# Optimization experiments

Hardware: AMD Instinct MI355X
Metric: run time of the kernel (lower is better)

## Reference

```python
import jax, jax.numpy as jnp
from jax import lax
import numpy as np

K = 3          # kernel_size
PAD = 1        # K // 2
MAX_OFFSET = 0.1
EPS = 1e-8


def setup_inputs() -> dict:
    key = jax.random.key(0)
    k0, k1, k2 = jax.random.split(key, 3)
    B, C, H, W = 4, 64, 256, 256
    Cmid = C // 4
    x = jax.random.normal(k0, (B, C, H, W), jnp.float32)
    # offset_predictor: Conv2d(C+9, C//4, 3, pad=1) -> LeakyReLU(0.2) -> Conv2d(C//4, 2, 3, pad=1) -> Tanh
    w1 = jax.random.normal(k1, (Cmid, C + K * K, 3, 3), jnp.float32) * 0.05
    b1 = jnp.zeros((Cmid,), jnp.float32)
    w2 = jax.random.normal(k2, (2, Cmid, 3, 3), jnp.float32) * 0.05
    b2 = jnp.zeros((2,), jnp.float32)
    return {"x": x, "w1": w1, "b1": b1, "w2": w2, "b2": b2}


def _conv2d(x, w, b):
    # NCHW, OIHW, stride 1, pad 1 (SAME for 3x3)
    out = lax.conv_general_dilated(x, w, (1, 1), ((PAD, PAD), (PAD, PAD)),
                                   dimension_numbers=("NCHW", "OIHW", "NCHW"))
    return out + b[None, :, None, None]


def _local_cosine_similarity(x):
    # F.unfold with zero padding: neighbors[k] at spatial shift (di-1, dj-1), row-major k = di*K + dj
    B, C, H, W = x.shape
    xp = jnp.pad(x, ((0, 0), (0, 0), (PAD, PAD), (PAD, PAD)))
    neighbors = jnp.stack([xp[:, :, di:di + H, dj:dj + W]
                           for di in range(K) for dj in range(K)], axis=2)  # (B,C,9,H,W)
    center = x[:, :, None, :, :]                                            # (B,C,1,H,W)
    numerator = jnp.sum(neighbors * center, axis=1)                         # (B,9,H,W)
    center_norm = jnp.sqrt(jnp.sum(x * x, axis=1)) + EPS                    # (B,H,W)
    neighbor_norm = jnp.sqrt(jnp.sum(neighbors * neighbors, axis=1)) + EPS  # (B,9,H,W)
    return numerator / (center_norm[:, None] * neighbor_norm)               # (B,9,H,W)


def _grid_sample_border(x, grid):
    # bilinear, padding_mode='border', align_corners=True; grid: (B,H,W,2) with (gx,gy) in [-1,1]
    B, C, H, W = x.shape
    ix = (grid[..., 0] + 1.0) * 0.5 * (W - 1)
    iy = (grid[..., 1] + 1.0) * 0.5 * (H - 1)
    ix = jnp.clip(ix, 0.0, W - 1)
    iy = jnp.clip(iy, 0.0, H - 1)
    x0f = jnp.floor(ix); y0f = jnp.floor(iy)
    wx = ix - x0f; wy = iy - y0f
    x0 = x0f.astype(jnp.int32); y0 = y0f.astype(jnp.int32)
    x1 = jnp.minimum(x0 + 1, W - 1); y1 = jnp.minimum(y0 + 1, H - 1)

    def gather(img, yy, xx):  # img (C,H,W), yy/xx (H,W) -> (C,H,W)
        return img[:, yy, xx]

    g = jax.vmap(gather)
    v00 = g(x, y0, x0); v01 = g(x, y0, x1)
    v10 = g(x, y1, x0); v11 = g(x, y1, x1)
    wx = wx[:, None]; wy = wy[:, None]  # broadcast over channel dim
    return ((1 - wy) * ((1 - wx) * v00 + wx * v01)
            + wy * ((1 - wx) * v10 + wx * v11))


def reference(x, w1, b1, w2, b2):
    B, C, H, W = x.shape
    sim = _local_cosine_similarity(x)                       # (B,9,H,W)
    features = jnp.concatenate([x, sim], axis=1)            # (B,C+9,H,W)
    h = _conv2d(features, w1, b1)
    h = jnp.where(h >= 0, h, 0.2 * h)                       # LeakyReLU(0.2)
    offset = jnp.tanh(_conv2d(h, w2, b2)) * MAX_OFFSET      # (B,2,H,W)
    gy, gx = jnp.meshgrid(jnp.linspace(-1.0, 1.0, H),
                          jnp.linspace(-1.0, 1.0, W), indexing="ij")
    base_grid = jnp.stack([gx, gy], axis=-1)[None]          # (1,H,W,2)
    offset_grid = base_grid + jnp.transpose(offset, (0, 2, 3, 1))
    return _grid_sample_border(x, offset_grid)
```

## Files before the change

kernel.cpp:

```cpp
#include <hip/hip_runtime.h>
#include <math.h>

#define B 4
#define C 64
#define H 256
#define W 256
#define CMID 16
#define CIN 73
#define HW (H*W)
#define NW (CIN*9*CMID)
#define XS_STRIDE 260
#define XSR 258
#define PLN 258

__global__ void transpose_w1_kernel(const float* __restrict__ w1, float* __restrict__ wt) {
    int tid = blockIdx.x * blockDim.x + threadIdx.x;
    if (tid >= NW) return;
    int co = tid & (CMID - 1);
    int rest = tid >> 4;
    int ci = rest / 9;
    int k = rest - ci * 9;
    wt[tid] = w1[(co * CIN + ci) * 9 + k];
}

__device__ __forceinline__ void read_patch9(const float* __restrict__ base, float v[9]) {
#pragma unroll
    for (int r = 0; r < 3; ++r) {
        v[r * 3 + 0] = base[r * XSR + 0];
        v[r * 3 + 1] = base[r * XSR + 1];
        v[r * 3 + 2] = base[r * XSR + 2];
    }
}

__global__ __launch_bounds__(256) void sim_kernel(const float* __restrict__ x,
                                                  float* __restrict__ sim) {
    __shared__ float xs[2][4][3 * XSR];

    int bid = blockIdx.x;
    int sb = (bid & 7) * 128 + (bid >> 3);
    int b = sb >> 8;
    int y = sb & 255;
    int tid = threadIdx.x;

    const float* xb = x + (size_t)b * C * HW;

    bool rv[3];
    long off[3];
#pragma unroll
    for (int j = 0; j < 3; ++j) {
        int grow = y - 1 + j;
        rv[j] = (grow >= 0) && (grow < H);
        off[j] = (long)grow * W + tid;
    }

    if (tid < 48) {
        int e = tid & 1;
        int r = (tid >> 1) % 3;
        int q = (tid >> 1) / 3;
        (&xs[0][0][0])[q * (3 * XSR) + r * XSR + (e ? 257 : 0)] = 0.f;
    }

    float dot[9], nsq[9];
    float csq = 0.f;
#pragma unroll
    for (int i = 0; i < 9; ++i) { dot[i] = nsq[i] = 0.f; }

    float p[12];
#pragma unroll
    for (int k = 0; k < 4; ++k)
#pragma unroll
        for (int j = 0; j < 3; ++j)
            p[k * 3 + j] = rv[j] ? xb[(size_t)k * HW + off[j]] : 0.f;

    int cur = 0;
#pragma unroll 1
    for (int cc = 0; cc < C; cc += 4) {
#pragma unroll
        for (int k = 0; k < 4; ++k)
#pragma unroll
            for (int j = 0; j < 3; ++j)
                xs[cur][k][j * XSR + 1 + tid] = p[k * 3 + j];
        __syncthreads();

        if (cc + 4 < C) {
#pragma unroll
            for (int k = 0; k < 4; ++k)
#pragma unroll
                for (int j = 0; j < 3; ++j)
                    p[k * 3 + j] = rv[j] ? xb[(size_t)(cc + 4 + k) * HW + off[j]] : 0.f;
        }

#pragma unroll
        for (int k = 0; k < 4; ++k) {
            float v[9];
            read_patch9(&xs[cur][k][tid], v);
            float cv = v[4];
            csq = fmaf(cv, cv, csq);
#pragma unroll
            for (int kk = 0; kk < 9; ++kk) {
                if (kk == 4) continue;
                dot[kk] = fmaf(cv, v[kk], dot[kk]);
                nsq[kk] = fmaf(v[kk], v[kk], nsq[kk]);
            }
        }
        cur ^= 1;
    }

    dot[4] = csq;
    nsq[4] = csq;
    float cn = sqrtf(csq) + 1e-8f;
    float* so = sim + (size_t)b * 9 * HW + (size_t)y * W + tid;
#pragma unroll
    for (int kk = 0; kk < 9; ++kk)
        so[(size_t)kk * HW] = dot[kk] / (cn * (sqrtf(nsq[kk]) + 1e-8f));
}

__device__ __forceinline__ void conv1_co4(const float* __restrict__ pl, int l,
                                          int aL, int aR,
                                          const float4 wv[9], float4 acc[2][4]) {
    float v[4][6];
#pragma unroll
    for (int r = 0; r < 4; ++r) {
        const float* rp = pl + r * PLN;
        v[r][1] = rp[l];
        v[r][2] = rp[64 + l];
        v[r][3] = rp[128 + l];
        v[r][4] = rp[192 + l];
        v[r][0] = rp[aL];
        v[r][5] = rp[aR];
    }
#pragma unroll
    for (int kr = 0; kr < 3; ++kr)
#pragma unroll
        for (int kc = 0; kc < 3; ++kc) {
            float4 w = wv[kr * 3 + kc];
#pragma unroll
            for (int rr = 0; rr < 2; ++rr)
#pragma unroll
                for (int cc = 0; cc < 4; ++cc) {
                    float a = v[rr + kr][cc + kc];
                    acc[rr][cc].x = fmaf(a, w.x, acc[rr][cc].x);
                    acc[rr][cc].y = fmaf(a, w.y, acc[rr][cc].y);
                    acc[rr][cc].z = fmaf(a, w.z, acc[rr][cc].z);
                    acc[rr][cc].w = fmaf(a, w.w, acc[rr][cc].w);
                }
        }
}

__global__ __launch_bounds__(256) void conv1_kernel(const float* __restrict__ x,
                                                    const float* __restrict__ sim,
                                                    const float* __restrict__ wt,
                                                    const float* __restrict__ b1,
                                                    float* __restrict__ h) {
    __shared__ float xs[2][2][4 * PLN];

    int tid = threadIdx.x;
    int l = tid & 63;
    int wid = tid >> 6;
    int bid = blockIdx.x;
    int sb = (bid & 7) * 64 + (bid >> 3);
    int b  = sb >> 7;
    int y0 = (sb & 127) << 1;

    int vz;
    asm volatile("v_mov_b32 %0, 0" : "=v"(vz));
    const float4* wq = (const float4*)wt + vz;

    const float* gx = x + (size_t)b * C * HW;
    const float* gs = sim + (size_t)b * 9 * HW;

    int grow = y0 - 1 + wid;
    bool rvw = (grow >= 0) && (grow < H);
    size_t goff = (size_t)grow * W + 4 * l;

    int aL = (l == 0)  ? 256 : 191 + l;
    int aR = (l == 63) ? 257 : l + 1;

    if (tid < 32) {
        int bu = tid >> 4, ch = (tid >> 3) & 1, r = (tid >> 1) & 3, e = tid & 1;
        xs[bu][ch][r * PLN + 256 + e] = 0.f;
    }

    float4 bias = ((const float4*)b1)[wid];
    float4 acc[2][4];
#pragma unroll
    for (int rr = 0; rr < 2; ++rr)
#pragma unroll
        for (int cc = 0; cc < 4; ++cc) acc[rr][cc] = bias;

    float4 wA[9], wB[9];
#pragma unroll
    for (int k = 0; k < 9; ++k) wA[k] = wq[k * 4 + wid];

    float4 p0 = make_float4(0.f, 0.f, 0.f, 0.f), p1 = p0;
    if (rvw) {
        p0 = *(const float4*)(gx + goff);
        p1 = *(const float4*)(gx + HW + goff);
    }

    int cur = 0;
#pragma unroll 1
    for (int cc2 = 0; cc2 < 72; cc2 += 2) {
        {
            float* d0 = &xs[cur][0][wid * PLN];
            d0[l] = p0.x; d0[64 + l] = p0.y; d0[128 + l] = p0.z; d0[192 + l] = p0.w;
            float* d1 = &xs[cur][1][wid * PLN];
            d1[l] = p1.x; d1[64 + l] = p1.y; d1[128 + l] = p1.z; d1[192 + l] = p1.w;
        }
        __syncthreads();

        {
            int ci = cc2 + 2;
            p0 = make_float4(0.f, 0.f, 0.f, 0.f);
            if (rvw)
                p0 = (ci < C) ? *(const float4*)(gx + (size_t)ci * HW + goff)
                              : *(const float4*)(gs + (size_t)(ci - C) * HW + goff);
            int cj = cc2 + 3;
            p1 = make_float4(0.f, 0.f, 0.f, 0.f);
            if (rvw && cj < CIN)
                p1 = (cj < C) ? *(const float4*)(gx + (size_t)cj * HW + goff)
                              : *(const float4*)(gs + (size_t)(cj - C) * HW + goff);
        }

#pragma unroll
        for (int k = 0; k < 9; ++k) wB[k] = wq[((cc2 + 1) * 9 + k) * 4 + wid];

        conv1_co4(&xs[cur][0][0], l, aL, aR, wA, acc);

#pragma unroll
        for (int k = 0; k < 9; ++k) wA[k] = wq[((cc2 + 2) * 9 + k) * 4 + wid];

        conv1_co4(&xs[cur][1][0], l, aL, aR, wB, acc);

        cur ^= 1;
    }

    {
        float* d0 = &xs[cur][0][wid * PLN];
        d0[l] = p0.x; d0[64 + l] = p0.y; d0[128 + l] = p0.z; d0[192 + l] = p0.w;
    }
    __syncthreads();
    conv1_co4(&xs[cur][0][0], l, aL, aR, wA, acc);

    float* ho = h + ((size_t)b * CMID + 4 * wid) * HW + (size_t)y0 * W + 4 * l;
#pragma unroll
    for (int rr = 0; rr < 2; ++rr)
#pragma unroll
        for (int j = 0; j < 4; ++j) {
            float4 o;
            o.x = ((const float*)&acc[rr][0])[j];
            o.y = ((const float*)&acc[rr][1])[j];
            o.z = ((const float*)&acc[rr][2])[j];
            o.w = ((const float*)&acc[rr][3])[j];
            o.x = o.x >= 0.f ? o.x : 0.2f * o.x;
            o.y = o.y >= 0.f ? o.y : 0.2f * o.y;
            o.z = o.z >= 0.f ? o.z : 0.2f * o.z;
            o.w = o.w >= 0.f ? o.w : 0.2f * o.w;
            *(float4*)(ho + (size_t)j * HW + (size_t)rr * W) = o;
        }
}

__device__ __forceinline__ void read_patch_lds(const float* __restrict__ xsbuf,
                                               int rl, int px, float v[3][4]) {
    const float* pb = xsbuf + rl * XS_STRIDE + px;
#pragma unroll
    for (int r = 0; r < 3; ++r) {
        float2 p0 = *(const float2*)(pb + r * XS_STRIDE);
        float2 p1 = *(const float2*)(pb + r * XS_STRIDE + 2);
        v[r][0] = p0.x; v[r][1] = p0.y; v[r][2] = p1.x; v[r][3] = p1.y;
    }
}

__global__ __launch_bounds__(256) void offset_kernel(const float* __restrict__ h,
                                                     const float* __restrict__ w2,
                                                     const float* __restrict__ b2,
                                                     float2* __restrict__ off_buf) {
    __shared__ float lw2[CMID * 9 * 2];
    __shared__ float xs[2][4 * XS_STRIDE];

    int tid = threadIdx.x;
    for (int i = tid; i < CMID * 9 * 2; i += 256) {
        int co = i & 1;
        int rest = i >> 1;
        int ci = rest / 9;
        int kk = rest - ci * 9;
        lw2[i] = w2[(co * CMID + ci) * 9 + kk];
    }

    int bid = blockIdx.x;
    int sb = (bid & 7) * 64 + (bid >> 3);
    int b  = sb >> 7;
    int y0 = (sb & 127) << 1;
    int srow = tid >> 6;
    int sx4  = (tid & 63) << 2;
    int rl = tid >> 7;
    int px = (tid & 127) << 1;
    int y  = y0 + rl;

    int grow = y0 - 1 + srow;
    bool gvalid = (grow >= 0) && (grow < H);
    const float* gh = h + (size_t)b * CMID * HW + (size_t)grow * W + sx4;

    if (tid < 16) {
        int bu = tid >> 3, r = (tid >> 1) & 3, e = (tid & 1) ? 257 : 0;
        xs[bu][r * XS_STRIDE + e] = 0.f;
    }

    float s0x = b2[0], s0y = b2[1], s1x = b2[0], s1y = b2[1];

    float4 r4 = make_float4(0.f, 0.f, 0.f, 0.f);
    if (gvalid) r4 = *(const float4*)gh;

    int cur = 0;
#pragma unroll 1
    for (int ci = 0; ci < CMID; ++ci) {
        float* dst = &xs[cur][srow * XS_STRIDE + 1 + sx4];
        dst[0] = r4.x; dst[1] = r4.y; dst[2] = r4.z; dst[3] = r4.w;
        __syncthreads();
        if (ci + 1 < CMID) {
            r4 = make_float4(0.f, 0.f, 0.f, 0.f);
            if (gvalid) r4 = *(const float4*)(gh + (size_t)(ci + 1) * HW);
        }
        float v[3][4];
        read_patch_lds(xs[cur], rl, px, v);
#pragma unroll
        for (int kr = 0; kr < 3; ++kr)
#pragma unroll
            for (int kc = 0; kc < 3; ++kc) {
                float2 wv = *(const float2*)(lw2 + (ci * 9 + kr * 3 + kc) * 2);
                s0x = fmaf(v[kr][kc],     wv.x, s0x);
                s0y = fmaf(v[kr][kc],     wv.y, s0y);
                s1x = fmaf(v[kr][kc + 1], wv.x, s1x);
                s1y = fmaf(v[kr][kc + 1], wv.y, s1y);
            }
        cur ^= 1;
    }

    float ix0 = (float)px       + 0.1f * tanhf(s0x) * (0.5f * (float)(W - 1));
    float iy0 = (float)y        + 0.1f * tanhf(s0y) * (0.5f * (float)(H - 1));
    float ix1 = (float)(px + 1) + 0.1f * tanhf(s1x) * (0.5f * (float)(W - 1));
    float iy1 = (float)y        + 0.1f * tanhf(s1y) * (0.5f * (float)(H - 1));
    ix0 = fminf(fmaxf(ix0, 0.f), (float)(W - 1));
    iy0 = fminf(fmaxf(iy0, 0.f), (float)(H - 1));
    ix1 = fminf(fmaxf(ix1, 0.f), (float)(W - 1));
    iy1 = fminf(fmaxf(iy1, 0.f), (float)(H - 1));

    float4* op = (float4*)(off_buf + (size_t)b * HW + (size_t)y * W + px);
    *op = make_float4(ix0, iy0, ix1, iy1);
}

#define SROWS 35
__global__ __launch_bounds__(256) void sample_kernel(const float* __restrict__ x,
                                                     const float2* __restrict__ off_buf,
                                                     float* __restrict__ out) {
    __shared__ float xs[SROWS * 256];

    int bid = blockIdx.x;
    int sb = (bid & 7) * 16 + (bid >> 3);
    int b  = sb >> 5;
    int ty = sb & 31;
    int cg = blockIdx.y;
    int tid = threadIdx.x;

    int ybase = ty << 3;
    int lo = ybase - 13;

    int a00[8], a01[8], a10[8], a11[8];
    float wx[8], wy[8];
    const float2* ob2 = off_buf + (size_t)b * HW + (size_t)ybase * W + tid;
#pragma unroll
    for (int r = 0; r < 8; ++r) {
        float2 o = ob2[r * W];
        float xf = floorf(o.x), yf = floorf(o.y);
        wx[r] = o.x - xf; wy[r] = o.y - yf;
        int x0 = (int)xf, yy0 = (int)yf;
        int x1 = min(x0 + 1, W - 1), yy1 = min(yy0 + 1, H - 1);
        int r0 = (yy0 - lo) << 8, r1 = (yy1 - lo) << 8;
        a00[r] = r0 + x0; a01[r] = r0 + x1;
        a10[r] = r1 + x0; a11[r] = r1 + x1;
    }

    const float* xb = x + ((size_t)b * C + cg * 4) * HW;
    float* outb = out + ((size_t)b * C + cg * 4) * HW + (size_t)ybase * W + tid;

#pragma unroll 1
    for (int c = 0; c < 4; ++c) {
        __syncthreads();
        const float* src = xb + (size_t)c * HW;
        for (int j = tid; j < SROWS * 64; j += 256) {
            int row = j >> 6, x4 = (j & 63) << 2;
            int grw = min(max(lo + row, 0), H - 1);
            *(float4*)&xs[(row << 8) + x4] = *(const float4*)(src + (size_t)grw * W + x4);
        }
        __syncthreads();
        float* oc = outb + (size_t)c * HW;
#pragma unroll
        for (int r = 0; r < 8; ++r) {
            float v00 = xs[a00[r]], v01 = xs[a01[r]];
            float v10 = xs[a10[r]], v11 = xs[a11[r]];
            float top = fmaf(wx[r], v01 - v00, v00);
            float bot = fmaf(wx[r], v11 - v10, v10);
            oc[r * W] = fmaf(wy[r], bot - top, top);
        }
    }
}

extern "C" void kernel_launch(void* const* d_in, const int* in_sizes, int n_in,
                              void* d_out, int out_size, void* d_ws, size_t ws_size,
                              hipStream_t stream) {
    const float* x  = (const float*)d_in[0];
    const float* w1 = (const float*)d_in[1];
    const float* b1 = (const float*)d_in[2];
    const float* w2 = (const float*)d_in[3];
    const float* b2 = (const float*)d_in[4];
    float* out = (float*)d_out;

    float* ws  = (float*)d_ws;
    float* wt  = ws;
    float* sim = ws + 16384;
    float* h   = sim + (size_t)B * 9 * HW;
    float2* off_buf = (float2*)(h + (size_t)B * CMID * HW);

    transpose_w1_kernel<<<(NW + 255) / 256, 256, 0, stream>>>(w1, wt);

    sim_kernel<<<B * H, 256, 0, stream>>>(x, sim);
    conv1_kernel<<<512, 256, 0, stream>>>(x, sim, wt, b1, h);
    offset_kernel<<<512, 256, 0, stream>>>(h, w2, b2, off_buf);
    sample_kernel<<<dim3(128, 16), 256, 0, stream>>>(x, off_buf, out);
}
```

Before: 238.8 us.

## Compute two output rows and two pixels per thread in sim kernel

The local cosine similarity kernel now has each block cover two output rows, with each thread producing two adjacent pixels. It loads four input rows per channel group instead of three, which cuts redundant global row loads from 3x to 2x. Shared memory holds even and odd columns in split halves so the paired neighbour reads avoid bank conflicts, and the results are stored as float2. Doubling the accumulators raises register pressure, and the grid shrinks from 1024 to 512 blocks.

```diff
diff --git a/kernel.cpp b/kernel.cpp
--- a/kernel.cpp
+++ b/kernel.cpp
@@ -10,8 +10,8 @@
 #define HW (H*W)
 #define NW (CIN*9*CMID)
 #define XS_STRIDE 260
-#define XSR 258
 #define PLN 258
+#define SE  258
 
 __global__ void transpose_w1_kernel(const float* __restrict__ w1, float* __restrict__ wt) {
     int tid = blockIdx.x * blockDim.x + threadIdx.x;
@@ -23,96 +23,111 @@
     wt[tid] = w1[(co * CIN + ci) * 9 + k];
 }
 
-__device__ __forceinline__ void read_patch9(const float* __restrict__ base, float v[9]) {
-#pragma unroll
-    for (int r = 0; r < 3; ++r) {
-        v[r * 3 + 0] = base[r * XSR + 0];
-        v[r * 3 + 1] = base[r * XSR + 1];
-        v[r * 3 + 2] = base[r * XSR + 2];
-    }
-}
-
 __global__ __launch_bounds__(256) void sim_kernel(const float* __restrict__ x,
                                                   float* __restrict__ sim) {
-    __shared__ float xs[2][4][3 * XSR];
+    __shared__ float xs[2][4][4 * SE];
 
     int bid = blockIdx.x;
-    int sb = (bid & 7) * 128 + (bid >> 3);
-    int b = sb >> 8;
-    int y = sb & 255;
+    int sb = (bid & 7) * 64 + (bid >> 3);
+    int b  = sb >> 7;
+    int y0 = (sb & 127) << 1;
     int tid = threadIdx.x;
+    int rl = tid >> 7;
+    int k  = tid & 127;
+    int px = k << 1;
+    int y  = y0 + rl;
+
+    int scol = (tid & 1) ? 130 + (tid >> 1) : (tid >> 1);
+
+    bool rv[4];
+    size_t off[4];
+#pragma unroll
+    for (int j = 0; j < 4; ++j) {
+        int grow = y0 - 1 + j;
+        rv[j] = (grow >= 0) && (grow < H);
+        off[j] = (size_t)grow * W + tid;
+    }
+
+    if (tid < 64) {
+        int e = tid & 1;
+        int r = (tid >> 1) & 3;
+        int q = tid >> 3;
+        (&xs[0][0][0])[q * (4 * SE) + r * SE + 128 + e] = 0.f;
+    }
+
+    float dot0[9], nsq0[9], dot1[9], nsq1[9];
+    float csq0 = 0.f, csq1 = 0.f;
+#pragma unroll
+    for (int i = 0; i < 9; ++i) { dot0[i] = dot1[i] = nsq0[i] = nsq1[i] = 0.f; }
 
     const float* xb = x + (size_t)b * C * HW;
-
-    bool rv[3];
-    long off[3];
-#pragma unroll
-    for (int j = 0; j < 3; ++j) {
-        int grow = y - 1 + j;
-        rv[j] = (grow >= 0) && (grow < H);
-        off[j] = (long)grow * W + tid;
-    }
-
-    if (tid < 48) {
-        int e = tid & 1;
-        int r = (tid >> 1) % 3;
-        int q = (tid >> 1) / 3;
-        (&xs[0][0][0])[q * (3 * XSR) + r * XSR + (e ? 257 : 0)] = 0.f;
-    }
-
-    float dot[9], nsq[9];
-    float csq = 0.f;
-#pragma unroll
-    for (int i = 0; i < 9; ++i) { dot[i] = nsq[i] = 0.f; }
-
-    float p[12];
-#pragma unroll
-    for (int k = 0; k < 4; ++k)
-#pragma unroll
-        for (int j = 0; j < 3; ++j)
-            p[k * 3 + j] = rv[j] ? xb[(size_t)k * HW + off[j]] : 0.f;
+    float p[16];
+#pragma unroll
+    for (int kk = 0; kk < 4; ++kk)
+#pragma unroll
+        for (int j = 0; j < 4; ++j)
+            p[kk * 4 + j] = rv[j] ? xb[(size_t)kk * HW + off[j]] : 0.f;
 
     int cur = 0;
 #pragma unroll 1
     for (int cc = 0; cc < C; cc += 4) {
 #pragma unroll
-        for (int k = 0; k < 4; ++k)
-#pragma unroll
-            for (int j = 0; j < 3; ++j)
-                xs[cur][k][j * XSR + 1 + tid] = p[k * 3 + j];
+        for (int kk = 0; kk < 4; ++kk)
+#pragma unroll
+            for (int j = 0; j < 4; ++j)
+                xs[cur][kk][j * SE + scol] = p[kk * 4 + j];
         __syncthreads();
 
         if (cc + 4 < C) {
 #pragma unroll
-            for (int k = 0; k < 4; ++k)
-#pragma unroll
-                for (int j = 0; j < 3; ++j)
-                    p[k * 3 + j] = rv[j] ? xb[(size_t)(cc + 4 + k) * HW + off[j]] : 0.f;
-        }
-
-#pragma unroll
-        for (int k = 0; k < 4; ++k) {
-            float v[9];
-            read_patch9(&xs[cur][k][tid], v);
-            float cv = v[4];
-            csq = fmaf(cv, cv, csq);
-#pragma unroll
-            for (int kk = 0; kk < 9; ++kk) {
-                if (kk == 4) continue;
-                dot[kk] = fmaf(cv, v[kk], dot[kk]);
-                nsq[kk] = fmaf(v[kk], v[kk], nsq[kk]);
+            for (int kk = 0; kk < 4; ++kk)
+#pragma unroll
+                for (int j = 0; j < 4; ++j)
+                    p[kk * 4 + j] = rv[j] ? xb[(size_t)(cc + 4 + kk) * HW + off[j]] : 0.f;
+        }
+
+#pragma unroll
+        for (int kk = 0; kk < 4; ++kk) {
+            const float* base = &xs[cur][kk][rl * SE];
+            float v[3][4];
+#pragma unroll
+            for (int r = 0; r < 3; ++r) {
+                const float* rp = base + r * SE;
+                v[r][0] = rp[129 + k];
+                v[r][1] = rp[k];
+                v[r][2] = rp[130 + k];
+                v[r][3] = rp[k + 1];
             }
+            float cv0 = v[1][1], cv1 = v[1][2];
+            csq0 = fmaf(cv0, cv0, csq0);
+            csq1 = fmaf(cv1, cv1, csq1);
+#pragma unroll
+            for (int kr = 0; kr < 3; ++kr)
+#pragma unroll
+                for (int kc = 0; kc < 3; ++kc) {
+                    int kk9 = kr * 3 + kc;
+                    if (kk9 == 4) continue;
+                    float n0 = v[kr][kc], n1 = v[kr][kc + 1];
+                    dot0[kk9] = fmaf(cv0, n0, dot0[kk9]);
+                    nsq0[kk9] = fmaf(n0, n0, nsq0[kk9]);
+                    dot1[kk9] = fmaf(cv1, n1, dot1[kk9]);
+                    nsq1[kk9] = fmaf(n1, n1, nsq1[kk9]);
+                }
         }
         cur ^= 1;
     }
 
-    dot[4] = csq;
-    nsq[4] = csq;
-    float cn = sqrtf(csq) + 1e-8f;
-    float* so = sim + (size_t)b * 9 * HW + (size_t)y * W + tid;
-#pragma unroll
-    for (int kk = 0; kk < 9; ++kk)
-        so[(size_t)kk * HW] = dot[kk] / (cn * (sqrtf(nsq[kk]) + 1e-8f));
+    dot0[4] = csq0; nsq0[4] = csq0;
+    dot1[4] = csq1; nsq1[4] = csq1;
+    float cn0 = sqrtf(csq0) + 1e-8f;
+    float cn1 = sqrtf(csq1) + 1e-8f;
+    float* so = sim + (size_t)b * 9 * HW + (size_t)y * W + px;
+#pragma unroll
+    for (int kk9 = 0; kk9 < 9; ++kk9) {
+        float s0 = dot0[kk9] / (cn0 * (sqrtf(nsq0[kk9]) + 1e-8f));
+        float s1 = dot1[kk9] / (cn1 * (sqrtf(nsq1[kk9]) + 1e-8f));
+        *(float2*)(so + (size_t)kk9 * HW) = make_float2(s0, s1);
+    }
 }
 
 __device__ __forceinline__ void conv1_co4(const float* __restrict__ pl, int l,
@@ -192,7 +207,8 @@
 #pragma unroll
     for (int k = 0; k < 9; ++k) wA[k] = wq[k * 4 + wid];
 
-    float4 p0 = make_float4(0.f, 0.f, 0.f, 0.f), p1 = p0;
+    const float4 z4 = make_float4(0.f, 0.f, 0.f, 0.f);
+    float4 p0 = z4, p1 = z4;
     if (rvw) {
         p0 = *(const float4*)(gx + goff);
         p1 = *(const float4*)(gx + HW + goff);
@@ -211,12 +227,12 @@
 
         {
             int ci = cc2 + 2;
-            p0 = make_float4(0.f, 0.f, 0.f, 0.f);
+            p0 = z4;
             if (rvw)
                 p0 = (ci < C) ? *(const float4*)(gx + (size_t)ci * HW + goff)
                               : *(const float4*)(gs + (size_t)(ci - C) * HW + goff);
             int cj = cc2 + 3;
-            p1 = make_float4(0.f, 0.f, 0.f, 0.f);
+            p1 = z4;
             if (rvw && cj < CIN)
                 p1 = (cj < C) ? *(const float4*)(gx + (size_t)cj * HW + goff)
                               : *(const float4*)(gs + (size_t)(cj - C) * HW + goff);
@@ -423,7 +439,7 @@
 
     transpose_w1_kernel<<<(NW + 255) / 256, 256, 0, stream>>>(w1, wt);
 
-    sim_kernel<<<B * H, 256, 0, stream>>>(x, sim);
+    sim_kernel<<<512, 256, 0, stream>>>(x, sim);
     conv1_kernel<<<512, 256, 0, stream>>>(x, sim, wt, b1, h);
     offset_kernel<<<512, 256, 0, stream>>>(h, w2, b2, off_buf);
     sample_kernel<<<dim3(128, 16), 256, 0, stream>>>(x, off_buf, out);
```

New measurement: 242.0 us. Within noise of the previous version (+1.4%).
